# Kernel optimization log

Hardware: AMD Instinct MI355X
Metric: run time of the kernel (lower is better)

Reference implementation:

```python
import jax, jax.numpy as jnp
import numpy as np

D_MODEL = 1024
NUM_EXPERTS = 8
TOP_K = 2


def setup_inputs() -> dict:
    key = jax.random.key(0)
    k_x, k_g, k_w1, k_w2 = jax.random.split(key, 4)
    B, S, D, E = 4, 2048, D_MODEL, NUM_EXPERTS
    s_in = 1.0 / np.sqrt(D)
    s_hid = 1.0 / np.sqrt(4 * D)
    return {
        "x": jax.random.normal(k_x, (B, S, D), dtype=jnp.float32),
        "gate_w": jax.random.uniform(k_g, (E, D), jnp.float32, -s_in, s_in),
        "w1": jax.random.uniform(k_w1, (E, 4 * D, D), jnp.float32, -s_in, s_in),
        "w2": jax.random.uniform(k_w2, (E, D, 4 * D), jnp.float32, -s_hid, s_hid),
    }


def reference(x, gate_w, w1, w2):
    # x: [B,S,D]; gate_w: [E,D]; w1: [E,4D,D]; w2: [E,D,4D]
    gate_logits = jnp.einsum("bsd,ed->bse", x, gate_w)  # [B,S,E]
    top_v, top_i = jax.lax.top_k(gate_logits, TOP_K)     # [B,S,K]
    gates = jax.nn.softmax(top_v, axis=-1)               # [B,S,K]
    # combine weights per expert: [B,S,E]
    combine = jnp.sum(
        jax.nn.one_hot(top_i, NUM_EXPERTS, dtype=x.dtype) * gates[..., None],
        axis=-2,
    )
    out = jnp.zeros_like(x)
    for e in range(NUM_EXPERTS):
        h = jax.nn.relu(jnp.einsum("bsd,fd->bsf", x, w1[e]))   # [B,S,4D]
        y = jnp.einsum("bsf,df->bsd", h, w2[e])                # [B,S,D]
        out = out + combine[..., e, None] * y
    return out
```

## Files before the change

kernel.cpp:

```cpp
#include <hip/hip_runtime.h>
#include <hip/hip_bf16.h>

#define D_MODEL 1024
#define HDIM    4096
#define NE      8

typedef __attribute__((ext_vector_type(8))) short short8;
typedef __attribute__((ext_vector_type(4))) float f32x4;
typedef __attribute__((ext_vector_type(2))) __bf16 bf16x2;
typedef __attribute__((ext_vector_type(4))) unsigned int uint4v;

__device__ inline unsigned pk2(float a, float b) {
  bf16x2 v; v[0] = (__bf16)a; v[1] = (__bf16)b;
  return __builtin_bit_cast(unsigned, v);
}
__device__ inline unsigned short f2bf(float a) {
  __bf16 v = (__bf16)a;
  return __builtin_bit_cast(unsigned short, v);
}

__global__ __launch_bounds__(256) void gate_kernel(
    const float* __restrict__ x, const float* __restrict__ gw,
    int* __restrict__ counts, int* __restrict__ tk_e, float* __restrict__ tk_g)
{
  const int t = blockIdx.x;
  const int tid = threadIdx.x;
  const float4 xv = ((const float4*)(x + (size_t)t * D_MODEL))[tid];
  float part[NE];
#pragma unroll
  for (int e = 0; e < NE; ++e) {
    const float4 gv = ((const float4*)(gw + e * D_MODEL))[tid];
    part[e] = xv.x * gv.x + xv.y * gv.y + xv.z * gv.z + xv.w * gv.w;
  }
#pragma unroll
  for (int off = 32; off > 0; off >>= 1)
#pragma unroll
    for (int e = 0; e < NE; ++e) part[e] += __shfl_down(part[e], off, 64);
  __shared__ float red[4][NE];
  const int wid = tid >> 6, lane = tid & 63;
  if (lane == 0)
    for (int e = 0; e < NE; ++e) red[wid][e] = part[e];
  __syncthreads();
  if (tid == 0) {
    float lg[NE];
    for (int e = 0; e < NE; ++e) lg[e] = red[0][e] + red[1][e] + red[2][e] + red[3][e];
    int e0 = 0;
    for (int e = 1; e < NE; ++e) if (lg[e] > lg[e0]) e0 = e;
    int e1 = (e0 == 0) ? 1 : 0;
    for (int e = 0; e < NE; ++e) { if (e == e0) continue; if (lg[e] > lg[e1]) e1 = e; }
    const float v0 = lg[e0], v1 = lg[e1];
    const float g0 = 1.0f / (1.0f + expf(v1 - v0));
    tk_e[2*t] = e0; tk_e[2*t+1] = e1;
    tk_g[2*t] = g0; tk_g[2*t+1] = 1.0f - g0;
    atomicAdd(&counts[e0], 1);
    atomicAdd(&counts[e1], 1);
  }
}

__global__ void prefix_kernel(const int* __restrict__ counts,
                              int* __restrict__ cursor, int* __restrict__ offsets) {
  if (threadIdx.x == 0) {
    int s = 0;
    for (int e = 0; e < NE; ++e) { offsets[e] = s; s += counts[e]; cursor[e] = 0; }
  }
}

__global__ __launch_bounds__(256) void place_kernel(
    const int* __restrict__ tk_e, const float* __restrict__ tk_g,
    const int* __restrict__ offsets, int* __restrict__ cursor,
    int* __restrict__ token_of, float* __restrict__ gate_of, int T)
{
  const int t = blockIdx.x * 256 + threadIdx.x;
  if (t >= T) return;
  for (int k = 0; k < 2; ++k) {
    const int e = tk_e[2*t + k];
    const int pos = offsets[e] + atomicAdd(&cursor[e], 1);
    token_of[pos] = t;
    gate_of[pos] = tk_g[2*t + k];
  }
}

__global__ __launch_bounds__(256) void gemm1_kernel(
    const float* __restrict__ x, const float* __restrict__ w1,
    const int* __restrict__ counts, const int* __restrict__ offsets,
    const int* __restrict__ token_of, unsigned short* __restrict__ h)
{
  const int e = blockIdx.y;
  const int ne = counts[e];
  const int zt = blockIdx.z;
  if (zt * 128 >= ne) return;
  const int off = offsets[e];
  const int p0 = off + zt * 128;
  const int pend = off + ne;
  const int f0 = blockIdx.x * 128;
  const float* __restrict__ w1e = w1 + (size_t)e * ((size_t)HDIM * D_MODEL);

  __shared__ __align__(16) short As[128][40];
  __shared__ __align__(16) short Bs[128][40];

  const int tid = threadIdx.x;
  const int r = tid >> 1, ch = tid & 1;
  const int p = p0 + r;
  const int pr = (p < pend) ? p : p0;
  const int tok = token_of[pr];
  const float* aptr = x + (size_t)tok * D_MODEL + ch * 16;
  const float* bptr = w1e + (size_t)(f0 + r) * D_MODEL + ch * 16;

  const int lane = tid & 63, wid = tid >> 6;
  const int wm = (wid & 1) * 64, wn = (wid >> 1) * 64;
  const int lr = lane & 15, lq = lane >> 4;

  f32x4 acc[4][4];
#pragma unroll
  for (int i = 0; i < 4; ++i)
#pragma unroll
    for (int j = 0; j < 4; ++j) acc[i][j] = (f32x4){0.f, 0.f, 0.f, 0.f};

  for (int kk = 0; kk < D_MODEL; kk += 32) {
    const float4 a0 = *(const float4*)(aptr + kk);
    const float4 a1 = *(const float4*)(aptr + kk + 4);
    const float4 a2 = *(const float4*)(aptr + kk + 8);
    const float4 a3 = *(const float4*)(aptr + kk + 12);
    const float4 b0 = *(const float4*)(bptr + kk);
    const float4 b1 = *(const float4*)(bptr + kk + 4);
    const float4 b2 = *(const float4*)(bptr + kk + 8);
    const float4 b3 = *(const float4*)(bptr + kk + 12);
    __syncthreads();
    uint4v wa0 = {pk2(a0.x,a0.y), pk2(a0.z,a0.w), pk2(a1.x,a1.y), pk2(a1.z,a1.w)};
    uint4v wa1 = {pk2(a2.x,a2.y), pk2(a2.z,a2.w), pk2(a3.x,a3.y), pk2(a3.z,a3.w)};
    uint4v wb0 = {pk2(b0.x,b0.y), pk2(b0.z,b0.w), pk2(b1.x,b1.y), pk2(b1.z,b1.w)};
    uint4v wb1 = {pk2(b2.x,b2.y), pk2(b2.z,b2.w), pk2(b3.x,b3.y), pk2(b3.z,b3.w)};
    *(uint4v*)&As[r][ch*16]     = wa0;
    *(uint4v*)&As[r][ch*16 + 8] = wa1;
    *(uint4v*)&Bs[r][ch*16]     = wb0;
    *(uint4v*)&Bs[r][ch*16 + 8] = wb1;
    __syncthreads();
    short8 af[4], bf8[4];
#pragma unroll
    for (int i = 0; i < 4; ++i) af[i]  = *(const short8*)&As[wm + i*16 + lr][lq*8];
#pragma unroll
    for (int j = 0; j < 4; ++j) bf8[j] = *(const short8*)&Bs[wn + j*16 + lr][lq*8];
#pragma unroll
    for (int i = 0; i < 4; ++i)
#pragma unroll
      for (int j = 0; j < 4; ++j)
        acc[i][j] = __builtin_amdgcn_mfma_f32_16x16x32_bf16(af[i], bf8[j], acc[i][j], 0, 0, 0);
  }

#pragma unroll
  for (int i = 0; i < 4; ++i) {
#pragma unroll
    for (int g = 0; g < 4; ++g) {
      const int m = wm + i*16 + lq*4 + g;
      const int pp = p0 + m;
      if (pp < pend) {
        unsigned short* hrow = h + (size_t)pp * HDIM + f0 + wn + lr;
#pragma unroll
        for (int j = 0; j < 4; ++j) {
          float v = acc[i][j][g];
          v = v > 0.f ? v : 0.f;
          hrow[j*16] = f2bf(v);
        }
      }
    }
  }
}

__global__ __launch_bounds__(256) void gemm2_kernel(
    const unsigned short* __restrict__ h, const float* __restrict__ w2,
    const int* __restrict__ counts, const int* __restrict__ offsets,
    const int* __restrict__ token_of, const float* __restrict__ gate_of,
    float* __restrict__ out)
{
  const int e = blockIdx.y;
  const int ne = counts[e];
  const int zt = blockIdx.z;
  if (zt * 128 >= ne) return;
  const int off = offsets[e];
  const int p0 = off + zt * 128;
  const int pend = off + ne;
  const int d0 = blockIdx.x * 128;
  const float* __restrict__ w2e = w2 + (size_t)e * ((size_t)D_MODEL * HDIM);

  __shared__ __align__(16) short As[128][40];
  __shared__ __align__(16) short Bs[128][40];

  const int tid = threadIdx.x;
  const int r = tid >> 1, ch = tid & 1;
  const int p = p0 + r;
  const int pr = (p < pend) ? p : p0;
  const unsigned short* aptr = h + (size_t)pr * HDIM + ch * 16;
  const float* bptr = w2e + (size_t)(d0 + r) * HDIM + ch * 16;

  const int lane = tid & 63, wid = tid >> 6;
  const int wm = (wid & 1) * 64, wn = (wid >> 1) * 64;
  const int lr = lane & 15, lq = lane >> 4;

  f32x4 acc[4][4];
#pragma unroll
  for (int i = 0; i < 4; ++i)
#pragma unroll
    for (int j = 0; j < 4; ++j) acc[i][j] = (f32x4){0.f, 0.f, 0.f, 0.f};

  for (int kk = 0; kk < HDIM; kk += 32) {
    const short8 av0 = *(const short8*)(aptr + kk);
    const short8 av1 = *(const short8*)(aptr + kk + 8);
    const float4 b0 = *(const float4*)(bptr + kk);
    const float4 b1 = *(const float4*)(bptr + kk + 4);
    const float4 b2 = *(const float4*)(bptr + kk + 8);
    const float4 b3 = *(const float4*)(bptr + kk + 12);
    __syncthreads();
    *(short8*)&As[r][ch*16]     = av0;
    *(short8*)&As[r][ch*16 + 8] = av1;
    uint4v wb0 = {pk2(b0.x,b0.y), pk2(b0.z,b0.w), pk2(b1.x,b1.y), pk2(b1.z,b1.w)};
    uint4v wb1 = {pk2(b2.x,b2.y), pk2(b2.z,b2.w), pk2(b3.x,b3.y), pk2(b3.z,b3.w)};
    *(uint4v*)&Bs[r][ch*16]     = wb0;
    *(uint4v*)&Bs[r][ch*16 + 8] = wb1;
    __syncthreads();
    short8 af[4], bf8[4];
#pragma unroll
    for (int i = 0; i < 4; ++i) af[i]  = *(const short8*)&As[wm + i*16 + lr][lq*8];
#pragma unroll
    for (int j = 0; j < 4; ++j) bf8[j] = *(const short8*)&Bs[wn + j*16 + lr][lq*8];
#pragma unroll
    for (int i = 0; i < 4; ++i)
#pragma unroll
      for (int j = 0; j < 4; ++j)
        acc[i][j] = __builtin_amdgcn_mfma_f32_16x16x32_bf16(af[i], bf8[j], acc[i][j], 0, 0, 0);
  }

#pragma unroll
  for (int i = 0; i < 4; ++i) {
#pragma unroll
    for (int g = 0; g < 4; ++g) {
      const int m = wm + i*16 + lq*4 + g;
      const int pp = p0 + m;
      if (pp < pend) {
        const int tok = token_of[pp];
        const float gv = gate_of[pp];
        float* orow = out + (size_t)tok * D_MODEL + d0 + wn + lr;
#pragma unroll
        for (int j = 0; j < 4; ++j)
          atomicAdd(&orow[j*16], gv * acc[i][j][g]);
      }
    }
  }
}

extern "C" void kernel_launch(void* const* d_in, const int* in_sizes, int n_in,
                              void* d_out, int out_size, void* d_ws, size_t ws_size,
                              hipStream_t stream)
{
  const float* x  = (const float*)d_in[0];
  const float* gw = (const float*)d_in[1];
  const float* w1 = (const float*)d_in[2];
  const float* w2 = (const float*)d_in[3];
  float* out = (float*)d_out;
  const int T = in_sizes[0] / D_MODEL;

  char* wsb = (char*)d_ws;
  int*   counts   = (int*)wsb;
  int*   cursor   = counts + 8;
  int*   offsets  = cursor + 8;
  int*   tk_e     = offsets + 8;
  float* tk_g     = (float*)(tk_e + 2*T);
  int*   token_of = (int*)(tk_g + 2*T);
  float* gate_of  = (float*)(token_of + 2*T);
  unsigned short* h = (unsigned short*)(wsb + (1u << 20));

  hipMemsetAsync(d_ws, 0, 96, stream);
  hipMemsetAsync(d_out, 0, (size_t)out_size * sizeof(float), stream);

  gate_kernel<<<T, 256, 0, stream>>>(x, gw, counts, tk_e, tk_g);
  prefix_kernel<<<1, 64, 0, stream>>>(counts, cursor, offsets);
  place_kernel<<<(T + 255) / 256, 256, 0, stream>>>(tk_e, tk_g, offsets, cursor,
                                                    token_of, gate_of, T);
  const int maxz = (T + 127) / 128;
  dim3 g1(HDIM / 128, NE, maxz);
  gemm1_kernel<<<g1, 256, 0, stream>>>(x, w1, counts, offsets, token_of, h);
  dim3 g2(D_MODEL / 128, NE, maxz);
  gemm2_kernel<<<g2, 256, 0, stream>>>(h, w2, counts, offsets, token_of, gate_of, out);
}
```

Before: 1.248 ms.

## Pre-convert x and weights to bf16 and stage GEMM tiles via direct-to-LDS loads

The gate kernel now also writes a bf16 copy of x. When the workspace is large enough, separate kernels convert w1 and w2 to bf16 inside the timed call. Both GEMMs then stage tiles with global_load_lds 16-byte async loads into unpadded LDS, and the grid order is swapped so token tiles vary fastest, which should improve weight reuse in L2. This removes the per-tile fp32 loads and packing in the GEMM loops, but adds a full weight conversion pass each call and drops the LDS padding, which risks bank conflicts.

```diff
diff --git a/kernel.cpp b/kernel.cpp
--- a/kernel.cpp
+++ b/kernel.cpp
@@ -1,5 +1,6 @@
 #include <hip/hip_runtime.h>
 #include <hip/hip_bf16.h>
+#include <stdint.h>
 
 #define D_MODEL 1024
 #define HDIM    4096
@@ -9,6 +10,7 @@
 typedef __attribute__((ext_vector_type(4))) float f32x4;
 typedef __attribute__((ext_vector_type(2))) __bf16 bf16x2;
 typedef __attribute__((ext_vector_type(4))) unsigned int uint4v;
+typedef __attribute__((ext_vector_type(2))) unsigned int uint2v;
 
 __device__ inline unsigned pk2(float a, float b) {
   bf16x2 v; v[0] = (__bf16)a; v[1] = (__bf16)b;
@@ -18,14 +20,24 @@
   __bf16 v = (__bf16)a;
   return __builtin_bit_cast(unsigned short, v);
 }
+__device__ inline void async16(const void* g, void* l) {
+  __builtin_amdgcn_global_load_lds(
+      (const __attribute__((address_space(1))) unsigned int*)g,
+      (__attribute__((address_space(3))) unsigned int*)l, 16, 0, 0);
+}
 
 __global__ __launch_bounds__(256) void gate_kernel(
     const float* __restrict__ x, const float* __restrict__ gw,
-    int* __restrict__ counts, int* __restrict__ tk_e, float* __restrict__ tk_g)
+    int* __restrict__ counts, int* __restrict__ tk_e, float* __restrict__ tk_g,
+    unsigned short* __restrict__ xbf)
 {
   const int t = blockIdx.x;
   const int tid = threadIdx.x;
   const float4 xv = ((const float4*)(x + (size_t)t * D_MODEL))[tid];
+  if (xbf) {
+    uint2v p; p[0] = pk2(xv.x, xv.y); p[1] = pk2(xv.z, xv.w);
+    ((uint2v*)(xbf + (size_t)t * D_MODEL))[tid] = p;
+  }
   float part[NE];
 #pragma unroll
   for (int e = 0; e < NE; ++e) {
@@ -48,8 +60,7 @@
     for (int e = 1; e < NE; ++e) if (lg[e] > lg[e0]) e0 = e;
     int e1 = (e0 == 0) ? 1 : 0;
     for (int e = 0; e < NE; ++e) { if (e == e0) continue; if (lg[e] > lg[e1]) e1 = e; }
-    const float v0 = lg[e0], v1 = lg[e1];
-    const float g0 = 1.0f / (1.0f + expf(v1 - v0));
+    const float g0 = 1.0f / (1.0f + expf(lg[e1] - lg[e0]));
     tk_e[2*t] = e0; tk_e[2*t+1] = e1;
     tk_g[2*t] = g0; tk_g[2*t+1] = 1.0f - g0;
     atomicAdd(&counts[e0], 1);
@@ -80,36 +91,73 @@
   }
 }
 
-__global__ __launch_bounds__(256) void gemm1_kernel(
-    const float* __restrict__ x, const float* __restrict__ w1,
+__global__ __launch_bounds__(256) void convert_kernel(
+    const float* __restrict__ src, unsigned short* __restrict__ dst, long n4)
+{
+  long i = (long)blockIdx.x * 256 + threadIdx.x;
+  const long stride = (long)gridDim.x * 256;
+  for (; i < n4; i += stride) {
+    const float4 v = ((const float4*)src)[i];
+    uint2v p; p[0] = pk2(v.x, v.y); p[1] = pk2(v.z, v.w);
+    ((uint2v*)dst)[i] = p;
+  }
+}
+
+template<bool ABF, bool BBF>
+__global__ __launch_bounds__(256) void gemm1_t(
+    const float* __restrict__ xf, const unsigned short* __restrict__ xb,
+    const float* __restrict__ w1f, const unsigned short* __restrict__ w1b,
     const int* __restrict__ counts, const int* __restrict__ offsets,
     const int* __restrict__ token_of, unsigned short* __restrict__ h)
 {
-  const int e = blockIdx.y;
+  const int e = blockIdx.z;
   const int ne = counts[e];
-  const int zt = blockIdx.z;
+  const int zt = blockIdx.x;
   if (zt * 128 >= ne) return;
   const int off = offsets[e];
-  const int p0 = off + zt * 128;
-  const int pend = off + ne;
-  const int f0 = blockIdx.x * 128;
-  const float* __restrict__ w1e = w1 + (size_t)e * ((size_t)HDIM * D_MODEL);
-
-  __shared__ __align__(16) short As[128][40];
-  __shared__ __align__(16) short Bs[128][40];
-
-  const int tid = threadIdx.x;
-  const int r = tid >> 1, ch = tid & 1;
-  const int p = p0 + r;
-  const int pr = (p < pend) ? p : p0;
-  const int tok = token_of[pr];
-  const float* aptr = x + (size_t)tok * D_MODEL + ch * 16;
-  const float* bptr = w1e + (size_t)(f0 + r) * D_MODEL + ch * 16;
-
-  const int lane = tid & 63, wid = tid >> 6;
+  const int p0 = off + zt * 128, pend = off + ne;
+  const int f0 = blockIdx.y * 128;
+
+  __shared__ __align__(16) short As[128 * 32];
+  __shared__ __align__(16) short Bs[128 * 32];
+
+  const int tid = threadIdx.x, lane = tid & 63, wid = tid >> 6;
   const int wm = (wid & 1) * 64, wn = (wid >> 1) * 64;
   const int lr = lane & 15, lq = lane >> 4;
 
+  const unsigned short* aSrc0 = nullptr; const unsigned short* aSrc1 = nullptr;
+  short* aDst0 = nullptr; short* aDst1 = nullptr;
+  const float* aptrF = nullptr;
+  if (ABF) {
+    const int r0 = wid * 32 + (lane >> 2), r1 = r0 + 16;
+    int i0 = p0 + r0; if (i0 >= pend) i0 = pend - 1;
+    int i1 = p0 + r1; if (i1 >= pend) i1 = pend - 1;
+    aSrc0 = xb + (size_t)token_of[i0] * D_MODEL + (lane & 3) * 8;
+    aSrc1 = xb + (size_t)token_of[i1] * D_MODEL + (lane & 3) * 8;
+    aDst0 = As + (wid * 2 + 0) * 512;
+    aDst1 = As + (wid * 2 + 1) * 512;
+  } else {
+    const int r = tid >> 1, ch = tid & 1;
+    int ip = p0 + r; if (ip >= pend) ip = pend - 1;
+    aptrF = xf + (size_t)token_of[ip] * D_MODEL + ch * 16;
+  }
+  const unsigned short* bSrc0 = nullptr; const unsigned short* bSrc1 = nullptr;
+  short* bDst0 = nullptr; short* bDst1 = nullptr;
+  const float* bptrF = nullptr;
+  if (BBF) {
+    const unsigned short* w1be = w1b + (size_t)e * ((size_t)HDIM * D_MODEL);
+    const int r0 = wid * 32 + (lane >> 2), r1 = r0 + 16;
+    bSrc0 = w1be + (size_t)(f0 + r0) * D_MODEL + (lane & 3) * 8;
+    bSrc1 = w1be + (size_t)(f0 + r1) * D_MODEL + (lane & 3) * 8;
+    bDst0 = Bs + (wid * 2 + 0) * 512;
+    bDst1 = Bs + (wid * 2 + 1) * 512;
+  } else {
+    const float* w1fe = w1f + (size_t)e * ((size_t)HDIM * D_MODEL);
+    const int r = tid >> 1, ch = tid & 1;
+    bptrF = w1fe + (size_t)(f0 + r) * D_MODEL + ch * 16;
+  }
+  const int rM = tid >> 1, chM = tid & 1;
+
   f32x4 acc[4][4];
 #pragma unroll
   for (int i = 0; i < 4; ++i)
@@ -117,34 +165,45 @@
     for (int j = 0; j < 4; ++j) acc[i][j] = (f32x4){0.f, 0.f, 0.f, 0.f};
 
   for (int kk = 0; kk < D_MODEL; kk += 32) {
-    const float4 a0 = *(const float4*)(aptr + kk);
-    const float4 a1 = *(const float4*)(aptr + kk + 4);
-    const float4 a2 = *(const float4*)(aptr + kk + 8);
-    const float4 a3 = *(const float4*)(aptr + kk + 12);
-    const float4 b0 = *(const float4*)(bptr + kk);
-    const float4 b1 = *(const float4*)(bptr + kk + 4);
-    const float4 b2 = *(const float4*)(bptr + kk + 8);
-    const float4 b3 = *(const float4*)(bptr + kk + 12);
+    float4 a0, a1, a2, a3, b0, b1, b2, b3;
+    if (!ABF) {
+      a0 = *(const float4*)(aptrF + kk);     a1 = *(const float4*)(aptrF + kk + 4);
+      a2 = *(const float4*)(aptrF + kk + 8); a3 = *(const float4*)(aptrF + kk + 12);
+    }
+    if (!BBF) {
+      b0 = *(const float4*)(bptrF + kk);     b1 = *(const float4*)(bptrF + kk + 4);
+      b2 = *(const float4*)(bptrF + kk + 8); b3 = *(const float4*)(bptrF + kk + 12);
+    }
     __syncthreads();
-    uint4v wa0 = {pk2(a0.x,a0.y), pk2(a0.z,a0.w), pk2(a1.x,a1.y), pk2(a1.z,a1.w)};
-    uint4v wa1 = {pk2(a2.x,a2.y), pk2(a2.z,a2.w), pk2(a3.x,a3.y), pk2(a3.z,a3.w)};
-    uint4v wb0 = {pk2(b0.x,b0.y), pk2(b0.z,b0.w), pk2(b1.x,b1.y), pk2(b1.z,b1.w)};
-    uint4v wb1 = {pk2(b2.x,b2.y), pk2(b2.z,b2.w), pk2(b3.x,b3.y), pk2(b3.z,b3.w)};
-    *(uint4v*)&As[r][ch*16]     = wa0;
-    *(uint4v*)&As[r][ch*16 + 8] = wa1;
-    *(uint4v*)&Bs[r][ch*16]     = wb0;
-    *(uint4v*)&Bs[r][ch*16 + 8] = wb1;
+    if (ABF) {
+      async16(aSrc0 + kk, aDst0);
+      async16(aSrc1 + kk, aDst1);
+    } else {
+      uint4v wa0 = {pk2(a0.x,a0.y), pk2(a0.z,a0.w), pk2(a1.x,a1.y), pk2(a1.z,a1.w)};
+      uint4v wa1 = {pk2(a2.x,a2.y), pk2(a2.z,a2.w), pk2(a3.x,a3.y), pk2(a3.z,a3.w)};
+      *(uint4v*)&As[rM * 32 + chM * 16]     = wa0;
+      *(uint4v*)&As[rM * 32 + chM * 16 + 8] = wa1;
+    }
+    if (BBF) {
+      async16(bSrc0 + kk, bDst0);
+      async16(bSrc1 + kk, bDst1);
+    } else {
+      uint4v wb0 = {pk2(b0.x,b0.y), pk2(b0.z,b0.w), pk2(b1.x,b1.y), pk2(b1.z,b1.w)};
+      uint4v wb1 = {pk2(b2.x,b2.y), pk2(b2.z,b2.w), pk2(b3.x,b3.y), pk2(b3.z,b3.w)};
+      *(uint4v*)&Bs[rM * 32 + chM * 16]     = wb0;
+      *(uint4v*)&Bs[rM * 32 + chM * 16 + 8] = wb1;
+    }
     __syncthreads();
-    short8 af[4], bf8[4];
-#pragma unroll
-    for (int i = 0; i < 4; ++i) af[i]  = *(const short8*)&As[wm + i*16 + lr][lq*8];
-#pragma unroll
-    for (int j = 0; j < 4; ++j) bf8[j] = *(const short8*)&Bs[wn + j*16 + lr][lq*8];
+    short8 af[4], bfr[4];
+#pragma unroll
+    for (int i = 0; i < 4; ++i) af[i]  = *(const short8*)&As[(wm + i*16 + lr) * 32 + lq * 8];
+#pragma unroll
+    for (int j = 0; j < 4; ++j) bfr[j] = *(const short8*)&Bs[(wn + j*16 + lr) * 32 + lq * 8];
 #pragma unroll
     for (int i = 0; i < 4; ++i)
 #pragma unroll
       for (int j = 0; j < 4; ++j)
-        acc[i][j] = __builtin_amdgcn_mfma_f32_16x16x32_bf16(af[i], bf8[j], acc[i][j], 0, 0, 0);
+        acc[i][j] = __builtin_amdgcn_mfma_f32_16x16x32_bf16(af[i], bfr[j], acc[i][j], 0, 0, 0);
   }
 
 #pragma unroll
@@ -166,36 +225,52 @@
   }
 }
 
-__global__ __launch_bounds__(256) void gemm2_kernel(
-    const unsigned short* __restrict__ h, const float* __restrict__ w2,
+template<bool BBF>
+__global__ __launch_bounds__(256) void gemm2_t(
+    const unsigned short* __restrict__ h, const float* __restrict__ w2f,
+    const unsigned short* __restrict__ w2b,
     const int* __restrict__ counts, const int* __restrict__ offsets,
     const int* __restrict__ token_of, const float* __restrict__ gate_of,
     float* __restrict__ out)
 {
-  const int e = blockIdx.y;
+  const int e = blockIdx.z;
   const int ne = counts[e];
-  const int zt = blockIdx.z;
+  const int zt = blockIdx.x;
   if (zt * 128 >= ne) return;
   const int off = offsets[e];
-  const int p0 = off + zt * 128;
-  const int pend = off + ne;
-  const int d0 = blockIdx.x * 128;
-  const float* __restrict__ w2e = w2 + (size_t)e * ((size_t)D_MODEL * HDIM);
-
-  __shared__ __align__(16) short As[128][40];
-  __shared__ __align__(16) short Bs[128][40];
-
-  const int tid = threadIdx.x;
-  const int r = tid >> 1, ch = tid & 1;
-  const int p = p0 + r;
-  const int pr = (p < pend) ? p : p0;
-  const unsigned short* aptr = h + (size_t)pr * HDIM + ch * 16;
-  const float* bptr = w2e + (size_t)(d0 + r) * HDIM + ch * 16;
-
-  const int lane = tid & 63, wid = tid >> 6;
+  const int p0 = off + zt * 128, pend = off + ne;
+  const int d0 = blockIdx.y * 128;
+
+  __shared__ __align__(16) short As[128 * 32];
+  __shared__ __align__(16) short Bs[128 * 32];
+
+  const int tid = threadIdx.x, lane = tid & 63, wid = tid >> 6;
   const int wm = (wid & 1) * 64, wn = (wid >> 1) * 64;
   const int lr = lane & 15, lq = lane >> 4;
 
+  const int rA0 = wid * 32 + (lane >> 2), rA1 = rA0 + 16;
+  int iA0 = p0 + rA0; if (iA0 >= pend) iA0 = pend - 1;
+  int iA1 = p0 + rA1; if (iA1 >= pend) iA1 = pend - 1;
+  const unsigned short* aSrc0 = h + (size_t)iA0 * HDIM + (lane & 3) * 8;
+  const unsigned short* aSrc1 = h + (size_t)iA1 * HDIM + (lane & 3) * 8;
+  short* aDst0 = As + (wid * 2 + 0) * 512;
+  short* aDst1 = As + (wid * 2 + 1) * 512;
+
+  const unsigned short* bSrc0 = nullptr; const unsigned short* bSrc1 = nullptr;
+  short* bDst0 = nullptr; short* bDst1 = nullptr;
+  const float* bptrF = nullptr;
+  if (BBF) {
+    const unsigned short* w2be = w2b + (size_t)e * ((size_t)D_MODEL * HDIM);
+    bSrc0 = w2be + (size_t)(d0 + rA0) * HDIM + (lane & 3) * 8;
+    bSrc1 = w2be + (size_t)(d0 + rA1) * HDIM + (lane & 3) * 8;
+    bDst0 = Bs + (wid * 2 + 0) * 512;
+    bDst1 = Bs + (wid * 2 + 1) * 512;
+  } else {
+    const float* w2fe = w2f + (size_t)e * ((size_t)D_MODEL * HDIM);
+    bptrF = w2fe + (size_t)(d0 + (tid >> 1)) * HDIM + (tid & 1) * 16;
+  }
+  const int rM = tid >> 1, chM = tid & 1;
+
   f32x4 acc[4][4];
 #pragma unroll
   for (int i = 0; i < 4; ++i)
@@ -203,30 +278,34 @@
     for (int j = 0; j < 4; ++j) acc[i][j] = (f32x4){0.f, 0.f, 0.f, 0.f};
 
   for (int kk = 0; kk < HDIM; kk += 32) {
-    const short8 av0 = *(const short8*)(aptr + kk);
-    const short8 av1 = *(const short8*)(aptr + kk + 8);
-    const float4 b0 = *(const float4*)(bptr + kk);
-    const float4 b1 = *(const float4*)(bptr + kk + 4);
-    const float4 b2 = *(const float4*)(bptr + kk + 8);
-    const float4 b3 = *(const float4*)(bptr + kk + 12);
+    float4 b0, b1, b2, b3;
+    if (!BBF) {
+      b0 = *(const float4*)(bptrF + kk);     b1 = *(const float4*)(bptrF + kk + 4);
+      b2 = *(const float4*)(bptrF + kk + 8); b3 = *(const float4*)(bptrF + kk + 12);
+    }
     __syncthreads();
-    *(short8*)&As[r][ch*16]     = av0;
-    *(short8*)&As[r][ch*16 + 8] = av1;
-    uint4v wb0 = {pk2(b0.x,b0.y), pk2(b0.z,b0.w), pk2(b1.x,b1.y), pk2(b1.z,b1.w)};
-    uint4v wb1 = {pk2(b2.x,b2.y), pk2(b2.z,b2.w), pk2(b3.x,b3.y), pk2(b3.z,b3.w)};
-    *(uint4v*)&Bs[r][ch*16]     = wb0;
-    *(uint4v*)&Bs[r][ch*16 + 8] = wb1;
+    async16(aSrc0 + kk, aDst0);
+    async16(aSrc1 + kk, aDst1);
+    if (BBF) {
+      async16(bSrc0 + kk, bDst0);
+      async16(bSrc1 + kk, bDst1);
+    } else {
+      uint4v wb0 = {pk2(b0.x,b0.y), pk2(b0.z,b0.w), pk2(b1.x,b1.y), pk2(b1.z,b1.w)};
+      uint4v wb1 = {pk2(b2.x,b2.y), pk2(b2.z,b2.w), pk2(b3.x,b3.y), pk2(b3.z,b3.w)};
+      *(uint4v*)&Bs[rM * 32 + chM * 16]     = wb0;
+      *(uint4v*)&Bs[rM * 32 + chM * 16 + 8] = wb1;
+    }
     __syncthreads();
-    short8 af[4], bf8[4];
-#pragma unroll
-    for (int i = 0; i < 4; ++i) af[i]  = *(const short8*)&As[wm + i*16 + lr][lq*8];
-#pragma unroll
-    for (int j = 0; j < 4; ++j) bf8[j] = *(const short8*)&Bs[wn + j*16 + lr][lq*8];
+    short8 af[4], bfr[4];
+#pragma unroll
+    for (int i = 0; i < 4; ++i) af[i]  = *(const short8*)&As[(wm + i*16 + lr) * 32 + lq * 8];
+#pragma unroll
+    for (int j = 0; j < 4; ++j) bfr[j] = *(const short8*)&Bs[(wn + j*16 + lr) * 32 + lq * 8];
 #pragma unroll
     for (int i = 0; i < 4; ++i)
 #pragma unroll
       for (int j = 0; j < 4; ++j)
-        acc[i][j] = __builtin_amdgcn_mfma_f32_16x16x32_bf16(af[i], bf8[j], acc[i][j], 0, 0, 0);
+        acc[i][j] = __builtin_amdgcn_mfma_f32_16x16x32_bf16(af[i], bfr[j], acc[i][j], 0, 0, 0);
   }
 
 #pragma unroll
@@ -266,18 +345,47 @@
   float* tk_g     = (float*)(tk_e + 2*T);
   int*   token_of = (int*)(tk_g + 2*T);
   float* gate_of  = (float*)(token_of + 2*T);
-  unsigned short* h = (unsigned short*)(wsb + (1u << 20));
+
+  const size_t MB = 1u << 20;
+  const size_t xbf_sz = (size_t)T * D_MODEL * 2;
+  const size_t wbf_sz = (size_t)NE * HDIM * D_MODEL * 2;
+  const size_t h_sz   = (size_t)(2*T) * HDIM * 2;
+
+  const bool tierB = ws_size >= MB + xbf_sz + h_sz;
+  const bool tierA = ws_size >= MB + xbf_sz + 2*wbf_sz + h_sz;
+
+  unsigned short* xbf = tierB ? (unsigned short*)(wsb + MB) : nullptr;
+  unsigned short* w1b = tierA ? (unsigned short*)(wsb + MB + xbf_sz) : nullptr;
+  unsigned short* w2b = tierA ? (unsigned short*)(wsb + MB + xbf_sz + wbf_sz) : nullptr;
+  unsigned short* h;
+  if (tierA)      h = (unsigned short*)(wsb + MB + xbf_sz + 2*wbf_sz);
+  else if (tierB) h = (unsigned short*)(wsb + MB + xbf_sz);
+  else            h = (unsigned short*)(wsb + MB);
 
   hipMemsetAsync(d_ws, 0, 96, stream);
   hipMemsetAsync(d_out, 0, (size_t)out_size * sizeof(float), stream);
 
-  gate_kernel<<<T, 256, 0, stream>>>(x, gw, counts, tk_e, tk_g);
+  gate_kernel<<<T, 256, 0, stream>>>(x, gw, counts, tk_e, tk_g, xbf);
   prefix_kernel<<<1, 64, 0, stream>>>(counts, cursor, offsets);
   place_kernel<<<(T + 255) / 256, 256, 0, stream>>>(tk_e, tk_g, offsets, cursor,
                                                     token_of, gate_of, T);
+  if (tierA) {
+    const long n4 = (long)NE * HDIM * D_MODEL / 4;
+    convert_kernel<<<4096, 256, 0, stream>>>(w1, w1b, n4);
+    convert_kernel<<<4096, 256, 0, stream>>>(w2, w2b, n4);
+  }
+
   const int maxz = (T + 127) / 128;
-  dim3 g1(HDIM / 128, NE, maxz);
-  gemm1_kernel<<<g1, 256, 0, stream>>>(x, w1, counts, offsets, token_of, h);
-  dim3 g2(D_MODEL / 128, NE, maxz);
-  gemm2_kernel<<<g2, 256, 0, stream>>>(h, w2, counts, offsets, token_of, gate_of, out);
-}
+  dim3 g1(maxz, HDIM / 128, NE);
+  dim3 g2(maxz, D_MODEL / 128, NE);
+  if (tierA) {
+    gemm1_t<true, true><<<g1, 256, 0, stream>>>(x, xbf, w1, w1b, counts, offsets, token_of, h);
+    gemm2_t<true><<<g2, 256, 0, stream>>>(h, w2, w2b, counts, offsets, token_of, gate_of, out);
+  } else if (tierB) {
+    gemm1_t<true, false><<<g1, 256, 0, stream>>>(x, xbf, w1, w1b, counts, offsets, token_of, h);
+    gemm2_t<false><<<g2, 256, 0, stream>>>(h, w2, w2b, counts, offsets, token_of, gate_of, out);
+  } else {
+    gemm1_t<false, false><<<g1, 256, 0, stream>>>(x, xbf, w1, w1b, counts, offsets, token_of, h);
+    gemm2_t<false><<<g2, 256, 0, stream>>>(h, w2, w2b, counts, offsets, token_of, gate_of, out);
+  }
+}
```

Result: no change. 1.262 ms (+1.2%).
